# Performance work log

Hardware: AMD Instinct MI355X
Metric: run time of the kernel (lower is better)

## Reference

```python
import jax, jax.numpy as jnp
import numpy as np

N_NODES = 20000
N_EDGES = 320000
FT_DIM = 128
N_HEADS = 8
HEAD_DIM = FT_DIM // N_HEADS


def setup_inputs() -> dict:
    key = jax.random.key(0)
    ks = jax.random.split(key, 8)
    nft = jax.random.normal(ks[0], (N_NODES, FT_DIM), dtype=jnp.float32)
    eft = jax.random.normal(ks[1], (N_EDGES, FT_DIM), dtype=jnp.float32)
    # path_encoding: Linear(3*ft_dim, ft_dim); stored as (in, out) for x @ W
    W_path = jax.random.normal(ks[2], (3 * FT_DIM, FT_DIM), dtype=jnp.float32) * (1.0 / np.sqrt(3 * FT_DIM))
    b_path = jnp.zeros((FT_DIM,), dtype=jnp.float32)
    # attn1: Linear(ft_dim, num_heads, bias=False), xavier_normal gain=1.414
    W_attn1 = jax.random.normal(ks[3], (FT_DIM, N_HEADS), dtype=jnp.float32) * (1.414 * np.sqrt(2.0 / (FT_DIM + N_HEADS)))
    attn2 = jax.random.normal(ks[4], (1, N_HEADS, HEAD_DIM), dtype=jnp.float32) * (1.414 * np.sqrt(2.0 / (N_HEADS + HEAD_DIM)))
    src = jax.random.randint(ks[5], (N_EDGES,), 0, N_NODES, dtype=jnp.int32)
    dst = jax.random.randint(ks[6], (N_EDGES,), 0, N_NODES, dtype=jnp.int32)
    return {"nft": nft, "eft": eft, "W_path": W_path, "b_path": b_path,
            "W_attn1": W_attn1, "attn2": attn2, "src": src, "dst": dst}


def reference(nft, eft, W_path, b_path, W_attn1, attn2, src, dst):
    E = eft.shape[0]
    N = nft.shape[0]
    hs = nft[src]                      # [E, F] gathered src node features
    hd = nft[dst]                      # [E, F] gathered dst node features
    # fused path-encoding MLP over [src || edge || dst]
    epaths = (jnp.concatenate([hs, eft, hd], axis=1) @ W_path + b_path)
    epaths = epaths.reshape(E, N_HEADS, HEAD_DIM)
    # per-edge attention logits
    a1 = hs @ W_attn1                  # [E, H]
    a2 = jnp.sum(epaths * attn2, axis=-1)  # [E, H]
    a = jax.nn.leaky_relu(a1 + a2)     # default negative_slope=0.01, matches F.leaky_relu
    # segment softmax over incoming edges of each dst node
    m = jax.ops.segment_max(a, dst, num_segments=N)  # [N, H]
    m = jnp.where(jnp.isfinite(m), m, 0.0)           # nodes w/o in-edges
    e = jnp.exp(a - m[dst])
    s = jax.ops.segment_sum(e, dst, num_segments=N)  # [N, H]
    att = e / s[dst]                   # [E, H]
    # weighted messages, scatter-sum to dst nodes
    msg = (epaths * att[:, :, None]).reshape(E, FT_DIM)
    agg = jax.ops.segment_sum(msg, dst, num_segments=N)  # [N, F]
    return jax.nn.relu(agg + nft)
```

## Files before the change

kernel.cpp:

```cpp
#include <hip/hip_runtime.h>
#include <hip/hip_bf16.h>

#define FT 128
#define NH 8

typedef short bf16x8 __attribute__((ext_vector_type(8)));
typedef ushort u16x8 __attribute__((ext_vector_type(8)));
typedef float f32x4 __attribute__((ext_vector_type(4)));

__device__ __forceinline__ ushort f2bf(float f) {
  __hip_bfloat16 h = __float2bfloat16(f);
  return *reinterpret_cast<ushort*>(&h);
}
__device__ __forceinline__ float bf2f(ushort u) {
  return __uint_as_float(((unsigned)u) << 16);
}

__global__ void k_setup(const float* __restrict__ Wp, const float* __restrict__ bp,
                        const float* __restrict__ at2, ushort* __restrict__ Wt1,
                        ushort* __restrict__ WtN, float* __restrict__ cb,
                        int* __restrict__ cnt, int N) {
  int i = blockIdx.x * 256 + threadIdx.x;
  if (i < N) cnt[i] = 0;
  if (i < 128 * 128) {
    int c = i >> 7, k = i & 127;
    Wt1[i] = f2bf(Wp[(size_t)(128 + k) * 128 + c]);
  }
  if (i < 256 * 128) {
    int c = i >> 7, k = i & 127;
    float v = (c < 128) ? Wp[(size_t)k * 128 + c]
                        : Wp[(size_t)(256 + k) * 128 + (c - 128)];
    WtN[i] = f2bf(v);
  }
  if (i < NH) {
    float s = 0.0f;
    #pragma unroll
    for (int j = 0; j < 16; ++j) s += bp[i * 16 + j] * at2[i * 16 + j];
    cb[i] = s;
  }
}

__global__ void k_hist(const int* __restrict__ dst, int* __restrict__ cnt, int E) {
  int e = blockIdx.x * 256 + threadIdx.x;
  if (e < E) atomicAdd(&cnt[dst[e]], 1);
}

__global__ void k_scan1(const int* __restrict__ cnt, int* __restrict__ bsum, int N) {
  int i = blockIdx.x * 256 + threadIdx.x;
  int v = (i < N) ? cnt[i] : 0;
  #pragma unroll
  for (int o = 1; o < 64; o <<= 1) v += __shfl_xor(v, o);
  __shared__ int ws[4];
  if ((threadIdx.x & 63) == 0) ws[threadIdx.x >> 6] = v;
  __syncthreads();
  if (threadIdx.x == 0) bsum[blockIdx.x] = ws[0] + ws[1] + ws[2] + ws[3];
}

__global__ __launch_bounds__(1024) void k_scan2(const int* __restrict__ bsum,
                                                int* __restrict__ boff,
                                                int* __restrict__ ptr, int nb, int N) {
  __shared__ int buf[1024];
  int t = threadIdx.x;
  int v = (t < nb) ? bsum[t] : 0;
  buf[t] = v;
  __syncthreads();
  #pragma unroll
  for (int o = 1; o < 1024; o <<= 1) {
    int x = (t >= o) ? buf[t - o] : 0;
    __syncthreads();
    buf[t] += x;
    __syncthreads();
  }
  if (t < nb) boff[t] = buf[t] - v;
  if (t == nb - 1) ptr[N] = buf[t];
}

__global__ void k_scan3(const int* __restrict__ cnt, const int* __restrict__ boff,
                        int* __restrict__ ptr, int* __restrict__ cur, int N) {
  int i = blockIdx.x * 256 + threadIdx.x;
  int v = (i < N) ? cnt[i] : 0;
  int lane = threadIdx.x & 63, wv = threadIdx.x >> 6;
  int s = v;
  #pragma unroll
  for (int o = 1; o < 64; o <<= 1) {
    int x = __shfl_up(s, o);
    if (lane >= o) s += x;
  }
  __shared__ int wsum[4];
  if (lane == 63) wsum[wv] = s;
  __syncthreads();
  int add = 0;
  for (int k = 0; k < wv; ++k) add += wsum[k];
  int exc = boff[blockIdx.x] + add + s - v;
  if (i < N) { ptr[i] = exc; cur[i] = exc; }
}

__global__ void k_fill(const int* __restrict__ dst, const int* __restrict__ src,
                       int* __restrict__ cur, int* __restrict__ pos,
                       int* __restrict__ srcS, int E) {
  int e = blockIdx.x * 256 + threadIdx.x;
  if (e < E) {
    int p = atomicAdd(&cur[dst[e]], 1);
    pos[e] = p;
    srcS[p] = src[e];
  }
}

__global__ __launch_bounds__(256) void k_node_mfma(
    const float* __restrict__ nft, const ushort* __restrict__ WtN,
    const float* __restrict__ at2, const float* __restrict__ Wa1,
    ushort* __restrict__ nsAll, float* __restrict__ c2n,
    float* __restrict__ a1n, int N)
{
  __shared__ ushort x[64][136];
  const int t = threadIdx.x;
  const int n0 = blockIdx.x * 64;

  #pragma unroll
  for (int r = 0; r < 4; ++r) {
    int idx = r * 2048 + t * 8;
    int ei = idx >> 7, c = idx & 127;
    const float* xr = nft + (size_t)min(n0 + ei, N - 1) * FT + c;
    float4 u = *(const float4*)xr;
    float4 v = *(const float4*)(xr + 4);
    u16x8 pk;
    pk[0] = f2bf(u.x); pk[1] = f2bf(u.y); pk[2] = f2bf(u.z); pk[3] = f2bf(u.w);
    pk[4] = f2bf(v.x); pk[5] = f2bf(v.y); pk[6] = f2bf(v.z); pk[7] = f2bf(v.w);
    *(u16x8*)&x[ei][c] = pk;
  }
  __syncthreads();

  const int w  = t >> 6;
  const int l  = t & 63;
  const int lr = l & 15;
  const int lk = l >> 4;

  bf16x8 breg[4][4];
  const ushort* wb = WtN + ((size_t)(w * 64 + lr) * 128 + lk * 8);
  #pragma unroll
  for (int ntl = 0; ntl < 4; ++ntl)
    #pragma unroll
    for (int ks = 0; ks < 4; ++ks)
      breg[ks][ntl] = *(const bf16x8*)(wb + (size_t)ntl * 16 * 128 + ks * 32);

  f32x4 acc[4][4];
  #pragma unroll
  for (int m = 0; m < 4; ++m)
    #pragma unroll
    for (int ntl = 0; ntl < 4; ++ntl) acc[m][ntl] = 0.0f;

  #pragma unroll
  for (int ks = 0; ks < 4; ++ks) {
    int kb = ks * 32 + lk * 8;
    #pragma unroll
    for (int m = 0; m < 4; ++m) {
      bf16x8 a = *(const bf16x8*)&x[m * 16 + lr][kb];
      #pragma unroll
      for (int ntl = 0; ntl < 4; ++ntl)
        acc[m][ntl] = __builtin_amdgcn_mfma_f32_16x16x32_bf16(a, breg[ks][ntl], acc[m][ntl], 0, 0, 0);
    }
  }

  #pragma unroll
  for (int ntl = 0; ntl < 4; ++ntl) {
    int col = w * 64 + ntl * 16 + lr;
    #pragma unroll
    for (int m = 0; m < 4; ++m) {
      int rb = m * 16 + lk * 4;
      f32x4 c = acc[m][ntl];
      #pragma unroll
      for (int r = 0; r < 4; ++r) {
        int node = n0 + rb + r;
        if (node < N) nsAll[(size_t)node * 256 + col] = f2bf(c[r]);
      }
      if (col >= 128) {
        int head = (col & 127) >> 4;
        float a2v = at2[col & 127];
        float s0 = c[0] * a2v, s1 = c[1] * a2v, s2 = c[2] * a2v, s3 = c[3] * a2v;
        #pragma unroll
        for (int off = 1; off < 16; off <<= 1) {
          s0 += __shfl_xor(s0, off);
          s1 += __shfl_xor(s1, off);
          s2 += __shfl_xor(s2, off);
          s3 += __shfl_xor(s3, off);
        }
        if (lr == 0) {
          float sa[4] = {s0, s1, s2, s3};
          #pragma unroll
          for (int r = 0; r < 4; ++r) {
            int node = n0 + rb + r;
            if (node < N) c2n[(size_t)node * NH + head] = sa[r];
          }
        }
      }
    }
  }

  {
    int ei = t >> 2, q = t & 3;
    int node = n0 + ei;
    if (node < N) {
      float a0 = 0.0f, a1 = 0.0f;
      for (int k = 0; k < FT; ++k) {
        float xv = bf2f(x[ei][k]);
        a0 = fmaf(xv, Wa1[k * NH + 2 * q], a0);
        a1 = fmaf(xv, Wa1[k * NH + 2 * q + 1], a1);
      }
      a1n[(size_t)node * NH + 2 * q]     = a0;
      a1n[(size_t)node * NH + 2 * q + 1] = a1;
    }
  }
}

__global__ __launch_bounds__(256) void k_edge_mfma(
    const float* __restrict__ eft, const ushort* __restrict__ Wt1,
    const int* __restrict__ pos, ushort* __restrict__ eps, int E)
{
  __shared__ ushort x[64][136];
  __shared__ ushort y[64][136];

  const int t = threadIdx.x;
  const int w  = t >> 6;
  const int l  = t & 63;
  const int lr = l & 15;
  const int lk = l >> 4;
  const int erow = t >> 4;
  const int ccol = (t & 15) * 8;

  bf16x8 breg[4][2];
  const ushort* wb = Wt1 + ((size_t)(w * 32 + lr) * 128 + lk * 8);
  #pragma unroll
  for (int ks = 0; ks < 4; ++ks) {
    breg[ks][0] = *(const bf16x8*)(wb + ks * 32);
    breg[ks][1] = *(const bf16x8*)(wb + 16 * 128 + ks * 32);
  }

  #pragma unroll
  for (int tile = 0; tile < 2; ++tile) {
    const int e0 = (blockIdx.x * 2 + tile) * 64;

    int pe[4];
    #pragma unroll
    for (int r = 0; r < 4; ++r) {
      int e = e0 + r * 16 + erow;
      pe[r] = (e < E) ? pos[e] : -1;
    }

    #pragma unroll
    for (int r = 0; r < 4; ++r) {
      int ei = r * 16 + erow;
      const float* ef = eft + (size_t)min(e0 + ei, E - 1) * FT + ccol;
      float4 u = *(const float4*)ef;
      float4 v = *(const float4*)(ef + 4);
      u16x8 pk;
      pk[0] = f2bf(u.x); pk[1] = f2bf(u.y); pk[2] = f2bf(u.z); pk[3] = f2bf(u.w);
      pk[4] = f2bf(v.x); pk[5] = f2bf(v.y); pk[6] = f2bf(v.z); pk[7] = f2bf(v.w);
      *(u16x8*)&x[ei][ccol] = pk;
    }
    __syncthreads();

    f32x4 acc[4][2];
    #pragma unroll
    for (int m = 0; m < 4; ++m) { acc[m][0] = 0.0f; acc[m][1] = 0.0f; }

    #pragma unroll
    for (int ks = 0; ks < 4; ++ks) {
      int kb = ks * 32 + lk * 8;
      #pragma unroll
      for (int m = 0; m < 4; ++m) {
        bf16x8 a = *(const bf16x8*)&x[m * 16 + lr][kb];
        acc[m][0] = __builtin_amdgcn_mfma_f32_16x16x32_bf16(a, breg[ks][0], acc[m][0], 0, 0, 0);
        acc[m][1] = __builtin_amdgcn_mfma_f32_16x16x32_bf16(a, breg[ks][1], acc[m][1], 0, 0, 0);
      }
    }

    #pragma unroll
    for (int ntl = 0; ntl < 2; ++ntl) {
      int col = w * 32 + ntl * 16 + lr;
      #pragma unroll
      for (int m = 0; m < 4; ++m) {
        int rb = m * 16 + lk * 4;
        f32x4 c = acc[m][ntl];
        y[rb + 0][col] = f2bf(c[0]);
        y[rb + 1][col] = f2bf(c[1]);
        y[rb + 2][col] = f2bf(c[2]);
        y[rb + 3][col] = f2bf(c[3]);
      }
    }
    __syncthreads();

    #pragma unroll
    for (int r = 0; r < 4; ++r) {
      int ei = r * 16 + erow;
      if (pe[r] >= 0) {
        u16x8 vv = *(const u16x8*)&y[ei][ccol];
        *(u16x8*)&eps[(size_t)pe[r] * FT + ccol] = vv;
      }
    }
  }
}

__global__ __launch_bounds__(256) void k_aggregate(
    const ushort* __restrict__ eps, const ushort* __restrict__ nsAll,
    const float* __restrict__ a1n, const float* __restrict__ c2n,
    const float* __restrict__ cb, const int* __restrict__ ptr,
    const int* __restrict__ srcS, const float* __restrict__ at2,
    const float* __restrict__ bp, const float* __restrict__ nft,
    float* __restrict__ out, int N)
{
  int wid = (blockIdx.x * 256 + threadIdx.x) >> 6;
  int l = threadIdx.x & 63;
  if (wid >= N) return;
  int beg = ptr[wid], end = ptr[wid + 1];
  int hh = l >> 3;
  float at0 = at2[l * 2], at1 = at2[l * 2 + 1];
  float c2b = c2n[(size_t)wid * NH + hh] + cb[hh];

  float m = -INFINITY, s = 0.0f, a0 = 0.0f, a1 = 0.0f;
  int i = beg;

  for (; i + 1 < end; i += 2) {
    int se0 = srcS[i];
    int se1 = srcS[i + 1];
    unsigned pe0 = *(const unsigned*)&eps[(size_t)i * FT + l * 2];
    unsigned pe1 = *(const unsigned*)&eps[(size_t)(i + 1) * FT + l * 2];
    unsigned pn0 = *(const unsigned*)&nsAll[(size_t)se0 * 256 + l * 2];
    unsigned pn1 = *(const unsigned*)&nsAll[(size_t)se1 * 256 + l * 2];
    float p00 = __uint_as_float(pe0 << 16)         + __uint_as_float(pn0 << 16);
    float p01 = __uint_as_float(pe0 & 0xFFFF0000u) + __uint_as_float(pn0 & 0xFFFF0000u);
    float p10 = __uint_as_float(pe1 << 16)         + __uint_as_float(pn1 << 16);
    float p11 = __uint_as_float(pe1 & 0xFFFF0000u) + __uint_as_float(pn1 & 0xFFFF0000u);
    float ce0 = p00 * at0 + p01 * at1;
    float ce1 = p10 * at0 + p11 * at1;
    ce0 += __shfl_xor(ce0, 1); ce1 += __shfl_xor(ce1, 1);
    ce0 += __shfl_xor(ce0, 2); ce1 += __shfl_xor(ce1, 2);
    ce0 += __shfl_xor(ce0, 4); ce1 += __shfl_xor(ce1, 4);
    float lin0 = a1n[(size_t)se0 * NH + hh] + ce0 + c2b;
    float lin1 = a1n[(size_t)se1 * NH + hh] + ce1 + c2b;
    float lv0 = lin0 > 0.0f ? lin0 : 0.01f * lin0;
    float lv1 = lin1 > 0.0f ? lin1 : 0.01f * lin1;
    float mn = fmaxf(m, fmaxf(lv0, lv1));
    float corr = __expf(m - mn);
    float e0 = __expf(lv0 - mn);
    float e1 = __expf(lv1 - mn);
    s  = s  * corr + e0 + e1;
    a0 = a0 * corr + e0 * p00 + e1 * p10;
    a1 = a1 * corr + e0 * p01 + e1 * p11;
    m = mn;
  }
  if (i < end) {
    int se = srcS[i];
    unsigned pe = *(const unsigned*)&eps[(size_t)i * FT + l * 2];
    unsigned pn = *(const unsigned*)&nsAll[(size_t)se * 256 + l * 2];
    float p0 = __uint_as_float(pe << 16)         + __uint_as_float(pn << 16);
    float p1 = __uint_as_float(pe & 0xFFFF0000u) + __uint_as_float(pn & 0xFFFF0000u);
    float ce = p0 * at0 + p1 * at1;
    ce += __shfl_xor(ce, 1);
    ce += __shfl_xor(ce, 2);
    ce += __shfl_xor(ce, 4);
    float lin = a1n[(size_t)se * NH + hh] + ce + c2b;
    float lv = lin > 0.0f ? lin : 0.01f * lin;
    float mn = fmaxf(m, lv);
    float corr = __expf(m - mn);
    float ev   = __expf(lv - mn);
    s  = s  * corr + ev;
    a0 = a0 * corr + ev * p0;
    a1 = a1 * corr + ev * p1;
    m = mn;
  }

  float2 nv = *(const float2*)&nft[(size_t)wid * FT + l * 2];
  float v0, v1;
  if (s > 0.0f) {
    float inv = 1.0f / s;
    unsigned pn2 = *(const unsigned*)&nsAll[(size_t)wid * 256 + 128 + l * 2];
    float2 bv = *(const float2*)&bp[l * 2];
    v0 = a0 * inv + __uint_as_float(pn2 << 16)         + bv.x + nv.x;
    v1 = a1 * inv + __uint_as_float(pn2 & 0xFFFF0000u) + bv.y + nv.y;
  } else {
    v0 = nv.x; v1 = nv.y;
  }
  float2 ov;
  ov.x = v0 > 0.0f ? v0 : 0.0f;
  ov.y = v1 > 0.0f ? v1 : 0.0f;
  *(float2*)&out[(size_t)wid * FT + l * 2] = ov;
}

extern "C" void kernel_launch(void* const* d_in, const int* in_sizes, int n_in,
                              void* d_out, int out_size, void* d_ws, size_t ws_size,
                              hipStream_t stream) {
  const float* nft = (const float*)d_in[0];
  const float* eft = (const float*)d_in[1];
  const float* Wp  = (const float*)d_in[2];
  const float* bp  = (const float*)d_in[3];
  const float* Wa1 = (const float*)d_in[4];
  const float* at2 = (const float*)d_in[5];
  const int*   src = (const int*)d_in[6];
  const int*   dst = (const int*)d_in[7];
  const int N = in_sizes[0] / FT;
  const int E = in_sizes[6];
  const int nb = (N + 255) / 256;

  char* ws = (char*)d_ws;
  size_t off = 0;
  ushort* eps = (ushort*)(ws + off);   off += (size_t)E * FT * sizeof(ushort);
  off = (off + 255) & ~(size_t)255;
  ushort* Wt1 = (ushort*)(ws + off);   off += (size_t)128 * 128 * sizeof(ushort);
  ushort* WtN = (ushort*)(ws + off);   off += (size_t)256 * 128 * sizeof(ushort);
  off = (off + 255) & ~(size_t)255;
  float* a1n = (float*)(ws + off);     off += (size_t)N * NH * sizeof(float);
  float* c2n = (float*)(ws + off);     off += (size_t)N * NH * sizeof(float);
  float* cb = (float*)(ws + off);      off += 256;
  ushort* nsAll = (ushort*)(ws + off); off += (size_t)N * 256 * sizeof(ushort);
  off = (off + 255) & ~(size_t)255;
  int* cnt = (int*)(ws + off);         off += (size_t)N * sizeof(int);
  int* ptr = (int*)(ws + off);         off += (size_t)(N + 1) * sizeof(int);
  int* cur = (int*)(ws + off);         off += (size_t)N * sizeof(int);
  int* bsum = (int*)(ws + off);        off += (size_t)nb * sizeof(int);
  int* boff = (int*)(ws + off);        off += (size_t)nb * sizeof(int);
  int* pos = (int*)(ws + off);         off += (size_t)E * sizeof(int);
  int* srcS = (int*)(ws + off);        off += (size_t)E * sizeof(int);

  int setup_n = (256 * 128 > N ? 256 * 128 : N);
  k_setup<<<(setup_n + 255) / 256, 256, 0, stream>>>(Wp, bp, at2, Wt1, WtN, cb, cnt, N);
  k_hist<<<(E + 255) / 256, 256, 0, stream>>>(dst, cnt, E);
  k_scan1<<<nb, 256, 0, stream>>>(cnt, bsum, N);
  k_scan2<<<1, 1024, 0, stream>>>(bsum, boff, ptr, nb, N);
  k_scan3<<<nb, 256, 0, stream>>>(cnt, boff, ptr, cur, N);
  k_fill<<<(E + 255) / 256, 256, 0, stream>>>(dst, src, cur, pos, srcS, E);

  k_node_mfma<<<(N + 63) / 64, 256, 0, stream>>>(nft, WtN, at2, Wa1, nsAll, c2n,
                                                 a1n, N);

  k_edge_mfma<<<(E + 127) / 128, 256, 0, stream>>>(eft, Wt1, pos, eps, E);

  k_aggregate<<<(N * 64 + 255) / 256, 256, 0, stream>>>(eps, nsAll, a1n, c2n, cb,
                                                        ptr, srcS, at2, bp,
                                                        nft, (float*)d_out, N);
}
```

Before: 150.4 us.

## Vectorize node attn LDS reads, double edge tiles per block, unroll aggregate by four

Three separate tweaks land together. The node kernel's attn1 dot product now reads eight bf16 values from shared memory per vector load. The edge MFMA kernel handles four 64-edge tiles per block instead of two, which halves the grid and spreads the register-resident weight load over more work. The aggregate kernel gains a 4-edge unrolled online-softmax loop so more gathers are in flight per iteration. The costs are more registers and fewer blocks in flight for the edge kernel.

```diff
diff --git a/kernel.cpp b/kernel.cpp
--- a/kernel.cpp
+++ b/kernel.cpp
@@ -201,10 +201,14 @@
     int node = n0 + ei;
     if (node < N) {
       float a0 = 0.0f, a1 = 0.0f;
-      for (int k = 0; k < FT; ++k) {
-        float xv = bf2f(x[ei][k]);
-        a0 = fmaf(xv, Wa1[k * NH + 2 * q], a0);
-        a1 = fmaf(xv, Wa1[k * NH + 2 * q + 1], a1);
+      for (int kb = 0; kb < FT; kb += 8) {
+        u16x8 xv8 = *(const u16x8*)&x[ei][kb];
+        #pragma unroll
+        for (int j = 0; j < 8; ++j) {
+          float xv = bf2f(xv8[j]);
+          a0 = fmaf(xv, Wa1[(kb + j) * NH + 2 * q], a0);
+          a1 = fmaf(xv, Wa1[(kb + j) * NH + 2 * q + 1], a1);
+        }
       }
       a1n[(size_t)node * NH + 2 * q]     = a0;
       a1n[(size_t)node * NH + 2 * q + 1] = a1;
@@ -236,8 +240,8 @@
   }
 
   #pragma unroll
-  for (int tile = 0; tile < 2; ++tile) {
-    const int e0 = (blockIdx.x * 2 + tile) * 64;
+  for (int tile = 0; tile < 4; ++tile) {
+    const int e0 = (blockIdx.x * 4 + tile) * 64;
 
     int pe[4];
     #pragma unroll
@@ -319,6 +323,54 @@
   float m = -INFINITY, s = 0.0f, a0 = 0.0f, a1 = 0.0f;
   int i = beg;
 
+  for (; i + 3 < end; i += 4) {
+    int se0 = srcS[i],     se1 = srcS[i + 1];
+    int se2 = srcS[i + 2], se3 = srcS[i + 3];
+    unsigned pe0 = *(const unsigned*)&eps[(size_t)i * FT + l * 2];
+    unsigned pe1 = *(const unsigned*)&eps[(size_t)(i + 1) * FT + l * 2];
+    unsigned pe2 = *(const unsigned*)&eps[(size_t)(i + 2) * FT + l * 2];
+    unsigned pe3 = *(const unsigned*)&eps[(size_t)(i + 3) * FT + l * 2];
+    unsigned pn0 = *(const unsigned*)&nsAll[(size_t)se0 * 256 + l * 2];
+    unsigned pn1 = *(const unsigned*)&nsAll[(size_t)se1 * 256 + l * 2];
+    unsigned pn2 = *(const unsigned*)&nsAll[(size_t)se2 * 256 + l * 2];
+    unsigned pn3 = *(const unsigned*)&nsAll[(size_t)se3 * 256 + l * 2];
+    float p00 = __uint_as_float(pe0 << 16)         + __uint_as_float(pn0 << 16);
+    float p01 = __uint_as_float(pe0 & 0xFFFF0000u) + __uint_as_float(pn0 & 0xFFFF0000u);
+    float p10 = __uint_as_float(pe1 << 16)         + __uint_as_float(pn1 << 16);
+    float p11 = __uint_as_float(pe1 & 0xFFFF0000u) + __uint_as_float(pn1 & 0xFFFF0000u);
+    float p20 = __uint_as_float(pe2 << 16)         + __uint_as_float(pn2 << 16);
+    float p21 = __uint_as_float(pe2 & 0xFFFF0000u) + __uint_as_float(pn2 & 0xFFFF0000u);
+    float p30 = __uint_as_float(pe3 << 16)         + __uint_as_float(pn3 << 16);
+    float p31 = __uint_as_float(pe3 & 0xFFFF0000u) + __uint_as_float(pn3 & 0xFFFF0000u);
+    float ce0 = p00 * at0 + p01 * at1;
+    float ce1 = p10 * at0 + p11 * at1;
+    float ce2 = p20 * at0 + p21 * at1;
+    float ce3 = p30 * at0 + p31 * at1;
+    ce0 += __shfl_xor(ce0, 1); ce1 += __shfl_xor(ce1, 1);
+    ce2 += __shfl_xor(ce2, 1); ce3 += __shfl_xor(ce3, 1);
+    ce0 += __shfl_xor(ce0, 2); ce1 += __shfl_xor(ce1, 2);
+    ce2 += __shfl_xor(ce2, 2); ce3 += __shfl_xor(ce3, 2);
+    ce0 += __shfl_xor(ce0, 4); ce1 += __shfl_xor(ce1, 4);
+    ce2 += __shfl_xor(ce2, 4); ce3 += __shfl_xor(ce3, 4);
+    float lin0 = a1n[(size_t)se0 * NH + hh] + ce0 + c2b;
+    float lin1 = a1n[(size_t)se1 * NH + hh] + ce1 + c2b;
+    float lin2 = a1n[(size_t)se2 * NH + hh] + ce2 + c2b;
+    float lin3 = a1n[(size_t)se3 * NH + hh] + ce3 + c2b;
+    float lv0 = lin0 > 0.0f ? lin0 : 0.01f * lin0;
+    float lv1 = lin1 > 0.0f ? lin1 : 0.01f * lin1;
+    float lv2 = lin2 > 0.0f ? lin2 : 0.01f * lin2;
+    float lv3 = lin3 > 0.0f ? lin3 : 0.01f * lin3;
+    float mn = fmaxf(fmaxf(m, fmaxf(lv0, lv1)), fmaxf(lv2, lv3));
+    float corr = __expf(m - mn);
+    float e0 = __expf(lv0 - mn);
+    float e1 = __expf(lv1 - mn);
+    float e2 = __expf(lv2 - mn);
+    float e3 = __expf(lv3 - mn);
+    s  = s  * corr + e0 + e1 + e2 + e3;
+    a0 = a0 * corr + e0 * p00 + e1 * p10 + e2 * p20 + e3 * p30;
+    a1 = a1 * corr + e0 * p01 + e1 * p11 + e2 * p21 + e3 * p31;
+    m = mn;
+  }
   for (; i + 1 < end; i += 2) {
     int se0 = srcS[i];
     int se1 = srcS[i + 1];
@@ -432,7 +484,7 @@
   k_node_mfma<<<(N + 63) / 64, 256, 0, stream>>>(nft, WtN, at2, Wa1, nsAll, c2n,
                                                  a1n, N);
 
-  k_edge_mfma<<<(E + 127) / 128, 256, 0, stream>>>(eft, Wt1, pos, eps, E);
+  k_edge_mfma<<<(E + 255) / 256, 256, 0, stream>>>(eft, Wt1, pos, eps, E);
 
   k_aggregate<<<(N * 64 + 255) / 256, 256, 0, stream>>>(eps, nsAll, a1n, c2n, cb,
                                                         ptr, srcS, at2, bp,
```

After: 149.8 us. About the same (-0.4%).
